# Kernel optimization log

Hardware: AMD Instinct MI355X
Metric: run time of the kernel (lower is better)

Reference implementation:

```python
import jax, jax.numpy as jnp
import numpy as np

B, NQ, NK, D, H, DK, DV, M = 1, 2048, 2048, 1024, 16, 64, 64, 64
EPS = 1e-5

def _layer_norm(x, gamma, beta):
    mu = jnp.mean(x, axis=-1, keepdims=True)
    var = jnp.mean(jnp.square(x - mu), axis=-1, keepdims=True)
    return (x - mu) * jax.lax.rsqrt(var + EPS) * gamma + beta

def setup_inputs() -> dict:
    key = jax.random.key(0)
    ks = jax.random.split(key, 16)
    s = 0.02  # xavier-ish init scale for 1024x1024 weights
    return {
        'queries': jax.random.normal(ks[0], (B, NQ, D), jnp.float32),
        'keys': jax.random.normal(ks[1], (B, NK, D), jnp.float32),
        'values': jax.random.normal(ks[2], (B, NK, D), jnp.float32),
        'attention_weights': jax.random.uniform(ks[3], (B, NQ, NK), jnp.float32),
        'prev_att': jax.random.normal(ks[4], (B, NQ, NK), jnp.float32) * 0.1,
        'attention_mask': jax.random.randint(ks[5], (B, NQ, NK), 0, 2).astype(bool),
        'Wq': jax.random.normal(ks[6], (H * DK, D), jnp.float32) * s,
        'bq': jnp.zeros((H * DK,), jnp.float32),
        'Wk': jax.random.normal(ks[7], (H * DK, D), jnp.float32) * s,
        'bk': jnp.zeros((H * DK,), jnp.float32),
        'Wv': jax.random.normal(ks[8], (H * DV, D), jnp.float32) * s,
        'bv': jnp.zeros((H * DV,), jnp.float32),
        'Wo': jax.random.normal(ks[9], (D, H * DV), jnp.float32) * s,
        'bo': jnp.zeros((D,), jnp.float32),
        'm_k': jax.random.normal(ks[10], (1, H, DK, M), jnp.float32) * s,  # stored pre-permuted as in module
        'm_v': jax.random.normal(ks[11], (1, H, M, DV), jnp.float32) * s,
        'gamma': jnp.ones((D,), jnp.float32),
        'beta': jnp.zeros((D,), jnp.float32),
    }

def reference(queries, keys, values, attention_weights, prev_att, attention_mask,
              Wq, bq, Wk, bk, Wv, bv, Wo, bo, m_k, m_v, gamma, beta):
    b, nq = queries.shape[:2]
    nk = keys.shape[1]
    # projections -> (b, h, nq, dk), (b, h, dk, nk), (b, h, nk, dv)
    q = (queries @ Wq.T + bq).reshape(b, nq, H, DK).transpose(0, 2, 1, 3)
    k = (keys @ Wk.T + bk).reshape(b, nk, H, DK).transpose(0, 2, 3, 1)
    v = (values @ Wv.T + bv).reshape(b, nk, H, DV).transpose(0, 2, 1, 3)
    # memory-slot concatenation
    k = jnp.concatenate([k, jnp.broadcast_to(m_k, (b, H, DK, M))], axis=3)   # (b,h,dk,nk+M)
    v = jnp.concatenate([v, jnp.broadcast_to(m_v, (b, H, M, DV))], axis=2)   # (b,h,nk+M,dv)
    aw = jnp.concatenate([attention_weights, jnp.ones((b, nq, M), attention_weights.dtype)], axis=-1)
    pa = jnp.concatenate([prev_att, jnp.zeros((b, nq, M), prev_att.dtype)], axis=-1)
    mask = jnp.concatenate([attention_mask, jnp.zeros((b, nq, M), bool)], axis=-1)
    # scores: scale, reweight, bias, mask (b_s==1 so rank-3 aw/pa broadcast over heads as in torch)
    att = jnp.einsum('bhqd,bhdn->bhqn', q, k) / np.sqrt(DK).astype(np.float32)
    att = att * aw + pa
    r_att = jnp.where(mask[:, None, :, :], -jnp.inf, att)
    p = jax.nn.softmax(r_att, axis=-1)  # dropout is identity (p=0 / eval)
    out = jnp.einsum('bhqn,bhnv->bqhv', p, v).reshape(b, nq, H * DV)
    out = out @ Wo.T + bo
    out = _layer_norm(queries + out, gamma, beta)  # use_res=True
    return out, r_att
```

## Files before the change

### kernel.cpp

```cpp
#include <hip/hip_runtime.h>
#include <hip/hip_bf16.h>
#include <math.h>

#define NQ 2048
#define NK 2048
#define DMODEL 1024
#define NHEAD 16
#define DK 64
#define DV 64
#define MSLOT 64
#define NKM (NK + MSLOT)
#define OUT_ELEMS (NQ * DMODEL)
#define RATT_ELEMS (NHEAD * NQ * NKM)

#define NEG_BIG (-1.0e30f)

#define LD4(p) (*(const float4*)(p))
#define ST4(p, v) (*(float4*)(p) = (v))

__device__ __forceinline__ void gemm64_body(
    const float* __restrict__ X, const float* __restrict__ W,
    const float* __restrict__ bias, float* __restrict__ C,
    int M, int N, int K, int bx, int by)
{
    __shared__ float Xs[32][68];
    __shared__ float Ws[32][68];
    const int t = threadIdx.x;
    const int ty = t >> 4, tx = t & 15;
    const int m0 = by * 64, n0 = bx * 64;
    float acc[4][4] = {};

    const int u = (t < 128) ? t : (t - 128);
    const int r4 = (u >> 3) * 4;
    const int c4 = u & 7;
    const float* src = (t < 128) ? &X[(size_t)(m0 + r4) * K + c4 * 4]
                                 : &W[(size_t)(n0 + r4) * K + c4 * 4];

    float4 v0, v1, v2, v3;
    v0 = LD4(src); v1 = LD4(src + K); v2 = LD4(src + 2 * K); v3 = LD4(src + 3 * K);

    for (int k0 = 0; k0 < K; k0 += 32) {
        __syncthreads();
        if (t < 128) {
            ST4(&Xs[c4 * 4 + 0][r4], make_float4(v0.x, v1.x, v2.x, v3.x));
            ST4(&Xs[c4 * 4 + 1][r4], make_float4(v0.y, v1.y, v2.y, v3.y));
            ST4(&Xs[c4 * 4 + 2][r4], make_float4(v0.z, v1.z, v2.z, v3.z));
            ST4(&Xs[c4 * 4 + 3][r4], make_float4(v0.w, v1.w, v2.w, v3.w));
        } else {
            ST4(&Ws[c4 * 4 + 0][r4], make_float4(v0.x, v1.x, v2.x, v3.x));
            ST4(&Ws[c4 * 4 + 1][r4], make_float4(v0.y, v1.y, v2.y, v3.y));
            ST4(&Ws[c4 * 4 + 2][r4], make_float4(v0.z, v1.z, v2.z, v3.z));
            ST4(&Ws[c4 * 4 + 3][r4], make_float4(v0.w, v1.w, v2.w, v3.w));
        }
        if (k0 + 32 < K) {
            const float* p = src + k0 + 32;
            v0 = LD4(p); v1 = LD4(p + K); v2 = LD4(p + 2 * K); v3 = LD4(p + 3 * K);
        }
        __syncthreads();
#pragma unroll 8
        for (int kk = 0; kk < 32; ++kk) {
            float a[4], b[4];
            *(float4*)&a[0] = LD4(&Xs[kk][ty * 4]);
            *(float4*)&b[0] = LD4(&Ws[kk][tx * 4]);
#pragma unroll
            for (int i = 0; i < 4; ++i)
#pragma unroll
                for (int j = 0; j < 4; ++j)
                    acc[i][j] += a[i] * b[j];
        }
    }
    float4 bv = LD4(&bias[n0 + tx * 4]);
#pragma unroll
    for (int i = 0; i < 4; ++i) {
        float4 o = make_float4(acc[i][0] + bv.x, acc[i][1] + bv.y,
                               acc[i][2] + bv.z, acc[i][3] + bv.w);
        ST4(&C[(size_t)(m0 + ty * 4 + i) * N + n0 + tx * 4], o);
    }
}

__global__ __launch_bounds__(256) void gemm64(
    const float* __restrict__ X, const float* __restrict__ W,
    const float* __restrict__ bias, float* __restrict__ C,
    int M, int N, int K)
{
    gemm64_body(X, W, bias, C, M, N, K, blockIdx.x, blockIdx.y);
}

__global__ __launch_bounds__(256) void qkv_gemm(
    const float* __restrict__ Xq, const float* __restrict__ Xk, const float* __restrict__ Xv,
    const float* __restrict__ Wq, const float* __restrict__ Wk, const float* __restrict__ Wv,
    const float* __restrict__ bq, const float* __restrict__ bk, const float* __restrict__ bv,
    float* __restrict__ Cq, float* __restrict__ Ck, float* __restrict__ Cv)
{
    const int z = blockIdx.z;
    const float* X = (z == 0) ? Xq : (z == 1) ? Xk : Xv;
    const float* W = (z == 0) ? Wq : (z == 1) ? Wk : Wv;
    const float* b = (z == 0) ? bq : (z == 1) ? bk : bv;
    float* C       = (z == 0) ? Cq : (z == 1) ? Ck : Cv;
    gemm64_body(X, W, b, C, NQ, DMODEL, DMODEL, blockIdx.x, blockIdx.y);
}

__global__ __launch_bounds__(256) void scores_main(
    const float* __restrict__ Q, const float* __restrict__ K,
    const float* __restrict__ AW, const float* __restrict__ PA,
    const unsigned char* __restrict__ MASK, float* __restrict__ Ratt)
{
    __shared__ float Qs[64][132];
    __shared__ float Ks[64][132];
    const int t = threadIdx.x;
    const int h = blockIdx.z;
    const int q0 = blockIdx.y * 128;
    const int n0 = blockIdx.x * 128;

#pragma unroll
    for (int i = 0; i < 2; ++i) {
        int idx = t + i * 256;
        int r = (idx >> 4) * 4, c4 = idx & 15;
        const float* p = &Q[(size_t)(q0 + r) * DMODEL + h * DK + c4 * 4];
        float4 v0 = LD4(p), v1 = LD4(p + DMODEL), v2 = LD4(p + 2 * DMODEL), v3 = LD4(p + 3 * DMODEL);
        ST4(&Qs[c4 * 4 + 0][r], make_float4(v0.x, v1.x, v2.x, v3.x));
        ST4(&Qs[c4 * 4 + 1][r], make_float4(v0.y, v1.y, v2.y, v3.y));
        ST4(&Qs[c4 * 4 + 2][r], make_float4(v0.z, v1.z, v2.z, v3.z));
        ST4(&Qs[c4 * 4 + 3][r], make_float4(v0.w, v1.w, v2.w, v3.w));
    }
#pragma unroll
    for (int i = 0; i < 2; ++i) {
        int idx = t + i * 256;
        int r = (idx >> 4) * 4, c4 = idx & 15;
        const float* p = &K[(size_t)(n0 + r) * DMODEL + h * DK + c4 * 4];
        float4 v0 = LD4(p), v1 = LD4(p + DMODEL), v2 = LD4(p + 2 * DMODEL), v3 = LD4(p + 3 * DMODEL);
        ST4(&Ks[c4 * 4 + 0][r], make_float4(v0.x, v1.x, v2.x, v3.x));
        ST4(&Ks[c4 * 4 + 1][r], make_float4(v0.y, v1.y, v2.y, v3.y));
        ST4(&Ks[c4 * 4 + 2][r], make_float4(v0.z, v1.z, v2.z, v3.z));
        ST4(&Ks[c4 * 4 + 3][r], make_float4(v0.w, v1.w, v2.w, v3.w));
    }
    __syncthreads();

    const int ty = t >> 4, tx = t & 15;
    float acc[8][8] = {};
#pragma unroll 4
    for (int kk = 0; kk < 64; ++kk) {
        float a[8], b[8];
        *(float4*)&a[0] = LD4(&Qs[kk][ty * 8]);
        *(float4*)&a[4] = LD4(&Qs[kk][ty * 8 + 4]);
        *(float4*)&b[0] = LD4(&Ks[kk][tx * 8]);
        *(float4*)&b[4] = LD4(&Ks[kk][tx * 8 + 4]);
#pragma unroll
        for (int i = 0; i < 8; ++i)
#pragma unroll
            for (int j = 0; j < 8; ++j)
                acc[i][j] += a[i] * b[j];
    }

#pragma unroll
    for (int i = 0; i < 8; ++i) {
        int q = q0 + ty * 8 + i;
        size_t mbase = (size_t)q * NK + n0 + tx * 8;
        size_t rbase = ((size_t)h * NQ + q) * NKM + n0 + tx * 8;
#pragma unroll
        for (int j4 = 0; j4 < 2; ++j4) {
            float4 aw = LD4(&AW[mbase + j4 * 4]);
            float4 pa = LD4(&PA[mbase + j4 * 4]);
            unsigned mm = *(const unsigned*)(MASK + mbase + j4 * 4);
            float4 o;
            o.x = (mm & 0x000000ffu) ? NEG_BIG : fmaf(acc[i][j4 * 4 + 0] * 0.125f, aw.x, pa.x);
            o.y = (mm & 0x0000ff00u) ? NEG_BIG : fmaf(acc[i][j4 * 4 + 1] * 0.125f, aw.y, pa.y);
            o.z = (mm & 0x00ff0000u) ? NEG_BIG : fmaf(acc[i][j4 * 4 + 2] * 0.125f, aw.z, pa.z);
            o.w = (mm & 0xff000000u) ? NEG_BIG : fmaf(acc[i][j4 * 4 + 3] * 0.125f, aw.w, pa.w);
            ST4(&Ratt[rbase + j4 * 4], o);
        }
    }
}

__global__ __launch_bounds__(256) void scores_mem(
    const float* __restrict__ Q, const float* __restrict__ mk,
    float* __restrict__ Ratt)
{
    __shared__ float Qs[64][132];
    __shared__ float Ks[64][68];
    const int t = threadIdx.x;
    const int h = blockIdx.y;
    const int q0 = blockIdx.x * 128;

#pragma unroll
    for (int i = 0; i < 2; ++i) {
        int idx = t + i * 256;
        int r = (idx >> 4) * 4, c4 = idx & 15;
        const float* p = &Q[(size_t)(q0 + r) * DMODEL + h * DK + c4 * 4];
        float4 v0 = LD4(p), v1 = LD4(p + DMODEL), v2 = LD4(p + 2 * DMODEL), v3 = LD4(p + 3 * DMODEL);
        ST4(&Qs[c4 * 4 + 0][r], make_float4(v0.x, v1.x, v2.x, v3.x));
        ST4(&Qs[c4 * 4 + 1][r], make_float4(v0.y, v1.y, v2.y, v3.y));
        ST4(&Qs[c4 * 4 + 2][r], make_float4(v0.z, v1.z, v2.z, v3.z));
        ST4(&Qs[c4 * 4 + 3][r], make_float4(v0.w, v1.w, v2.w, v3.w));
    }
#pragma unroll
    for (int i = 0; i < 4; ++i) {
        int idx = t + i * 256;
        int dk = idx >> 4, c4 = idx & 15;
        ST4(&Ks[dk][c4 * 4], LD4(&mk[((size_t)h * DK + dk) * MSLOT + c4 * 4]));
    }
    __syncthreads();

    const int ty = t >> 4, tx = t & 15;
    float acc[8][4] = {};
#pragma unroll 4
    for (int kk = 0; kk < 64; ++kk) {
        float a[8], b[4];
        *(float4*)&a[0] = LD4(&Qs[kk][ty * 8]);
        *(float4*)&a[4] = LD4(&Qs[kk][ty * 8 + 4]);
        *(float4*)&b[0] = LD4(&Ks[kk][tx * 4]);
#pragma unroll
        for (int i = 0; i < 8; ++i)
#pragma unroll
            for (int j = 0; j < 4; ++j)
                acc[i][j] += a[i] * b[j];
    }
#pragma unroll
    for (int i = 0; i < 8; ++i) {
        int q = q0 + ty * 8 + i;
        float4 o = make_float4(acc[i][0] * 0.125f, acc[i][1] * 0.125f,
                               acc[i][2] * 0.125f, acc[i][3] * 0.125f);
        ST4(&Ratt[((size_t)h * NQ + q) * NKM + NK + tx * 4], o);
    }
}

__global__ __launch_bounds__(256) void stats_kernel(
    const float* __restrict__ Ratt, float* __restrict__ stats)
{
    const int w = threadIdx.x >> 6, lane = threadIdx.x & 63;
    const int row = blockIdx.x * 4 + w;
    const float* r = Ratt + (size_t)row * NKM;
    float4 v[9];
#pragma unroll
    for (int i = 0; i < 8; ++i) v[i] = LD4(&r[i * 256 + lane * 4]);
    v[8] = (lane < 16) ? LD4(&r[2048 + lane * 4])
                       : make_float4(NEG_BIG, NEG_BIG, NEG_BIG, NEG_BIG);
    float m = NEG_BIG;
#pragma unroll
    for (int i = 0; i < 9; ++i)
        m = fmaxf(fmaxf(fmaxf(m, v[i].x), fmaxf(v[i].y, v[i].z)), v[i].w);
#pragma unroll
    for (int o = 32; o > 0; o >>= 1) m = fmaxf(m, __shfl_xor(m, o));
    float s = 0.f;
#pragma unroll
    for (int i = 0; i < 9; ++i)
        s += expf(v[i].x - m) + expf(v[i].y - m) + expf(v[i].z - m) + expf(v[i].w - m);
#pragma unroll
    for (int o = 32; o > 0; o >>= 1) s += __shfl_xor(s, o);
    if (lane == 0) { stats[row * 2] = m; stats[row * 2 + 1] = 1.f / s; }
}

__global__ __launch_bounds__(256) void pv_kernel(
    const float* __restrict__ Ratt, const float* __restrict__ stats,
    const float* __restrict__ V, const float* __restrict__ mv,
    float* __restrict__ AO)
{
    __shared__ float Ps[32][68];
    __shared__ float Vs[32][68];
    const int t = threadIdx.x;
    const int h = blockIdx.y;
    const int q0 = blockIdx.x * 64;
    const int ty = t >> 4, tx = t & 15;
    const int r2 = (t >> 3) * 2;
    const int n4 = t & 7;
    const int vn0 = t >> 4;
    const int vc = t & 15;

    float sm0, si0, sm1, si1;
    {
        int row = h * NQ + q0 + r2;
        sm0 = stats[row * 2];     si0 = stats[row * 2 + 1];
        sm1 = stats[row * 2 + 2]; si1 = stats[row * 2 + 3];
    }

    const float* rp = &Ratt[((size_t)h * NQ + q0 + r2) * NKM + n4 * 4];

    float4 r0 = LD4(rp), r1 = LD4(rp + NKM);
    float4 w0 = LD4(&V[(size_t)vn0 * DMODEL + h * DV + vc * 4]);
    float4 w1 = LD4(&V[(size_t)(vn0 + 16) * DMODEL + h * DV + vc * 4]);

    float acc[4][4] = {};
    for (int nc = 0; nc < NKM; nc += 32) {
        float e0x = expf(r0.x - sm0) * si0, e1x = expf(r1.x - sm1) * si1;
        float e0y = expf(r0.y - sm0) * si0, e1y = expf(r1.y - sm1) * si1;
        float e0z = expf(r0.z - sm0) * si0, e1z = expf(r1.z - sm1) * si1;
        float e0w = expf(r0.w - sm0) * si0, e1w = expf(r1.w - sm1) * si1;

        if (nc + 32 < NKM) {
            const float* p = rp + nc + 32;
            r0 = LD4(p); r1 = LD4(p + NKM);
        }

        __syncthreads();
        *(float2*)&Ps[n4 * 4 + 0][r2] = make_float2(e0x, e1x);
        *(float2*)&Ps[n4 * 4 + 1][r2] = make_float2(e0y, e1y);
        *(float2*)&Ps[n4 * 4 + 2][r2] = make_float2(e0z, e1z);
        *(float2*)&Ps[n4 * 4 + 3][r2] = make_float2(e0w, e1w);
        ST4(&Vs[vn0][vc * 4], w0);
        ST4(&Vs[vn0 + 16][vc * 4], w1);

        if (nc + 32 < NKM) {
            int ng0 = nc + 32 + vn0;
            int ng1 = nc + 32 + vn0 + 16;
            const float* vp0 = (ng0 < NK) ? &V[(size_t)ng0 * DMODEL + h * DV + vc * 4]
                                          : &mv[((size_t)h * MSLOT + (ng0 - NK)) * DV + vc * 4];
            const float* vp1 = (ng1 < NK) ? &V[(size_t)ng1 * DMODEL + h * DV + vc * 4]
                                          : &mv[((size_t)h * MSLOT + (ng1 - NK)) * DV + vc * 4];
            w0 = LD4(vp0); w1 = LD4(vp1);
        }
        __syncthreads();

#pragma unroll 8
        for (int kk = 0; kk < 32; ++kk) {
            float a[4], b[4];
            *(float4*)&a[0] = LD4(&Ps[kk][ty * 4]);
            *(float4*)&b[0] = LD4(&Vs[kk][tx * 4]);
#pragma unroll
            for (int i = 0; i < 4; ++i)
#pragma unroll
                for (int j = 0; j < 4; ++j)
                    acc[i][j] += a[i] * b[j];
        }
    }
#pragma unroll
    for (int i = 0; i < 4; ++i)
        ST4(&AO[(size_t)(q0 + ty * 4 + i) * DMODEL + h * DV + tx * 4],
            make_float4(acc[i][0], acc[i][1], acc[i][2], acc[i][3]));
}

__global__ __launch_bounds__(256) void ln_kernel(
    const float* __restrict__ Xres, const float* __restrict__ T,
    const float* __restrict__ gamma, const float* __restrict__ beta,
    float* __restrict__ out)
{
    const int row = blockIdx.x;
    const int t = threadIdx.x;
    const int w = t >> 6, lane = t & 63;
    __shared__ float red1[4], red2[4];

    float4 x = LD4(&Xres[(size_t)row * DMODEL + t * 4]);
    float4 tv = LD4(&T[(size_t)row * DMODEL + t * 4]);
    float v0 = x.x + tv.x, v1 = x.y + tv.y, v2 = x.z + tv.z, v3 = x.w + tv.w;

    float s = v0 + v1 + v2 + v3;
#pragma unroll
    for (int o = 32; o > 0; o >>= 1) s += __shfl_xor(s, o);
    if (lane == 0) red1[w] = s;
    __syncthreads();
    float mu = (red1[0] + red1[1] + red1[2] + red1[3]) * (1.f / DMODEL);

    float d0 = v0 - mu, d1 = v1 - mu, d2 = v2 - mu, d3 = v3 - mu;
    float vs = d0 * d0 + d1 * d1 + d2 * d2 + d3 * d3;
#pragma unroll
    for (int o = 32; o > 0; o >>= 1) vs += __shfl_xor(vs, o);
    if (lane == 0) red2[w] = vs;
    __syncthreads();
    float inv = rsqrtf((red2[0] + red2[1] + red2[2] + red2[3]) * (1.f / DMODEL) + 1e-5f);

    float4 g = LD4(&gamma[t * 4]);
    float4 bb = LD4(&beta[t * 4]);
    float4 o4 = make_float4(d0 * inv * g.x + bb.x, d1 * inv * g.y + bb.y,
                            d2 * inv * g.z + bb.z, d3 * inv * g.w + bb.w);
    ST4(&out[(size_t)row * DMODEL + t * 4], o4);
}

extern "C" void kernel_launch(void* const* d_in, const int* in_sizes, int n_in,
                              void* d_out, int out_size, void* d_ws, size_t ws_size,
                              hipStream_t stream) {
    const float* queries = (const float*)d_in[0];
    const float* keys    = (const float*)d_in[1];
    const float* values  = (const float*)d_in[2];
    const float* AW      = (const float*)d_in[3];
    const float* PA      = (const float*)d_in[4];
    const unsigned char* MASK = (const unsigned char*)d_in[5];
    const float* Wq = (const float*)d_in[6];  const float* bq = (const float*)d_in[7];
    const float* Wk = (const float*)d_in[8];  const float* bk = (const float*)d_in[9];
    const float* Wv = (const float*)d_in[10]; const float* bv = (const float*)d_in[11];
    const float* Wo = (const float*)d_in[12]; const float* bo = (const float*)d_in[13];
    const float* mk = (const float*)d_in[14]; const float* mv = (const float*)d_in[15];
    const float* gamma = (const float*)d_in[16]; const float* beta = (const float*)d_in[17];

    float* out  = (float*)d_out;
    float* ratt = out + OUT_ELEMS;

    float* ws = (float*)d_ws;
    float* Qp    = ws;
    float* Kp    = ws + 1 * OUT_ELEMS;
    float* Vp    = ws + 2 * OUT_ELEMS;
    float* AO    = ws + 3 * OUT_ELEMS;
    float* T     = ws + 4 * OUT_ELEMS;
    float* stats = ws + 5 * OUT_ELEMS;

    qkv_gemm<<<dim3(DMODEL / 64, NQ / 64, 3), 256, 0, stream>>>(
        queries, keys, values, Wq, Wk, Wv, bq, bk, bv, Qp, Kp, Vp);

    scores_main<<<dim3(NK / 128, NQ / 128, NHEAD), 256, 0, stream>>>(
        Qp, Kp, AW, PA, MASK, ratt);
    scores_mem<<<dim3(NQ / 128, NHEAD), 256, 0, stream>>>(Qp, mk, ratt);

    stats_kernel<<<(NHEAD * NQ) / 4, 256, 0, stream>>>(ratt, stats);

    pv_kernel<<<dim3(NQ / 64, NHEAD), 256, 0, stream>>>(ratt, stats, Vp, mv, AO);

    gemm64<<<dim3(DMODEL / 64, NQ / 64), 256, 0, stream>>>(
        AO, Wo, bo, T, NQ, DMODEL, DMODEL);

    ln_kernel<<<NQ, 256, 0, stream>>>(queries, T, gamma, beta, out);
}
```

Measured before the change: 951.4 us.

## Use bf16 MFMA for scores and PV, fuse partial softmax stats into scores

The QKV projection now writes bf16 outputs. The QK^T scores and P·V products move from scalar FP32 FMA to bf16 MFMA 16x16x32 instructions, with a new kernel that pre-transposes V into bf16. The scores kernels now emit per-tile row max and sum partials, so the separate stats pass reduces only 33 partials per row instead of rereading the whole score matrix. This removes a full read of the large r_att tensor and moves the matmul work onto matrix cores, at the cost of bf16 rounding in Q, K, V and P, which may affect accuracy.

```diff
diff --git a/kernel.cpp b/kernel.cpp
--- a/kernel.cpp
+++ b/kernel.cpp
@@ -1,5 +1,4 @@
 #include <hip/hip_runtime.h>
-#include <hip/hip_bf16.h>
 #include <math.h>
 
 #define NQ 2048
@@ -11,23 +10,44 @@
 #define MSLOT 64
 #define NKM (NK + MSLOT)
 #define OUT_ELEMS (NQ * DMODEL)
-#define RATT_ELEMS (NHEAD * NQ * NKM)
 
 #define NEG_BIG (-1.0e30f)
 
 #define LD4(p) (*(const float4*)(p))
 #define ST4(p, v) (*(float4*)(p) = (v))
 
-__device__ __forceinline__ void gemm64_body(
-    const float* __restrict__ X, const float* __restrict__ W,
-    const float* __restrict__ bias, float* __restrict__ C,
-    int M, int N, int K, int bx, int by)
-{
+using bfx8 = __attribute__((ext_vector_type(8))) short;
+using fx4  = __attribute__((ext_vector_type(4))) float;
+
+static __device__ __forceinline__ unsigned short f2bf(float f) {
+    union { float f; unsigned u; } v; v.f = f;
+    unsigned r = v.u + 0x7fffu + ((v.u >> 16) & 1u);
+    return (unsigned short)(r >> 16);
+}
+static __device__ __forceinline__ float bf2f(unsigned short u) {
+    union { unsigned u; float f; } v; v.u = (unsigned)u << 16;
+    return v.f;
+}
+
+__global__ __launch_bounds__(256) void qkv_gemm(
+    const float* __restrict__ Xq, const float* __restrict__ Xk, const float* __restrict__ Xv,
+    const float* __restrict__ Wq, const float* __restrict__ Wk, const float* __restrict__ Wv,
+    const float* __restrict__ bq, const float* __restrict__ bk, const float* __restrict__ bv,
+    unsigned short* __restrict__ Qb, unsigned short* __restrict__ Kb,
+    unsigned short* __restrict__ Vb)
+{
+    const int z = blockIdx.z;
+    const float* X = (z == 0) ? Xq : (z == 1) ? Xk : Xv;
+    const float* W = (z == 0) ? Wq : (z == 1) ? Wk : Wv;
+    const float* bias = (z == 0) ? bq : (z == 1) ? bk : bv;
+    unsigned short* O = (z == 0) ? Qb : (z == 1) ? Kb : Vb;
+
     __shared__ float Xs[32][68];
     __shared__ float Ws[32][68];
     const int t = threadIdx.x;
     const int ty = t >> 4, tx = t & 15;
-    const int m0 = by * 64, n0 = bx * 64;
+    const int m0 = blockIdx.y * 64, n0 = blockIdx.x * 64;
+    const int K = DMODEL;
     float acc[4][4] = {};
 
     const int u = (t < 128) ? t : (t - 128);
@@ -36,8 +56,7 @@
     const float* src = (t < 128) ? &X[(size_t)(m0 + r4) * K + c4 * 4]
                                  : &W[(size_t)(n0 + r4) * K + c4 * 4];
 
-    float4 v0, v1, v2, v3;
-    v0 = LD4(src); v1 = LD4(src + K); v2 = LD4(src + 2 * K); v3 = LD4(src + 3 * K);
+    float4 v0 = LD4(src), v1 = LD4(src + K), v2 = LD4(src + 2 * K), v3 = LD4(src + 3 * K);
 
     for (int k0 = 0; k0 < K; k0 += 32) {
         __syncthreads();
@@ -69,112 +88,108 @@
                     acc[i][j] += a[i] * b[j];
         }
     }
-    float4 bv = LD4(&bias[n0 + tx * 4]);
+    float4 bv4 = LD4(&bias[n0 + tx * 4]);
 #pragma unroll
     for (int i = 0; i < 4; ++i) {
-        float4 o = make_float4(acc[i][0] + bv.x, acc[i][1] + bv.y,
-                               acc[i][2] + bv.z, acc[i][3] + bv.w);
-        ST4(&C[(size_t)(m0 + ty * 4 + i) * N + n0 + tx * 4], o);
-    }
-}
-
-__global__ __launch_bounds__(256) void gemm64(
-    const float* __restrict__ X, const float* __restrict__ W,
-    const float* __restrict__ bias, float* __restrict__ C,
-    int M, int N, int K)
-{
-    gemm64_body(X, W, bias, C, M, N, K, blockIdx.x, blockIdx.y);
-}
-
-__global__ __launch_bounds__(256) void qkv_gemm(
-    const float* __restrict__ Xq, const float* __restrict__ Xk, const float* __restrict__ Xv,
-    const float* __restrict__ Wq, const float* __restrict__ Wk, const float* __restrict__ Wv,
-    const float* __restrict__ bq, const float* __restrict__ bk, const float* __restrict__ bv,
-    float* __restrict__ Cq, float* __restrict__ Ck, float* __restrict__ Cv)
-{
-    const int z = blockIdx.z;
-    const float* X = (z == 0) ? Xq : (z == 1) ? Xk : Xv;
-    const float* W = (z == 0) ? Wq : (z == 1) ? Wk : Wv;
-    const float* b = (z == 0) ? bq : (z == 1) ? bk : bv;
-    float* C       = (z == 0) ? Cq : (z == 1) ? Ck : Cv;
-    gemm64_body(X, W, b, C, NQ, DMODEL, DMODEL, blockIdx.x, blockIdx.y);
-}
-
-__global__ __launch_bounds__(256) void scores_main(
-    const float* __restrict__ Q, const float* __restrict__ K,
+        ushort4 o;
+        o.x = f2bf(acc[i][0] + bv4.x);
+        o.y = f2bf(acc[i][1] + bv4.y);
+        o.z = f2bf(acc[i][2] + bv4.z);
+        o.w = f2bf(acc[i][3] + bv4.w);
+        *(ushort4*)(O + (size_t)(m0 + ty * 4 + i) * DMODEL + n0 + tx * 4) = o;
+    }
+}
+
+__global__ __launch_bounds__(256) void vt_prep(
+    const unsigned short* __restrict__ Vb, const float* __restrict__ mv,
+    unsigned short* __restrict__ Vt)
+{
+    __shared__ unsigned short L[64][72];
+    const int c = blockIdx.x;
+    const int h = blockIdx.y;
+    const int t = threadIdx.x;
+    const int rn = t >> 2;
+    const int g4 = t & 3;
+
+    if (c < 32) {
+        const unsigned short* p = Vb + (size_t)(c * 64 + rn) * DMODEL + h * DV + g4 * 16;
+#pragma unroll
+        for (int e = 0; e < 16; ++e) L[rn][g4 * 16 + e] = p[e];
+    } else {
+        const float* p = mv + ((size_t)h * MSLOT + rn) * DV + g4 * 16;
+#pragma unroll
+        for (int e = 0; e < 16; ++e) L[rn][g4 * 16 + e] = f2bf(p[e]);
+    }
+    __syncthreads();
+    const int dv = rn;
+    unsigned short* q = Vt + ((size_t)h * DV + dv) * NKM + c * 64 + g4 * 16;
+#pragma unroll
+    for (int e = 0; e < 16; ++e) q[e] = L[g4 * 16 + e][dv];
+}
+
+__global__ __launch_bounds__(256) void scores_mfma(
+    const unsigned short* __restrict__ Qb, const unsigned short* __restrict__ Kb,
     const float* __restrict__ AW, const float* __restrict__ PA,
-    const unsigned char* __restrict__ MASK, float* __restrict__ Ratt)
-{
-    __shared__ float Qs[64][132];
-    __shared__ float Ks[64][132];
-    const int t = threadIdx.x;
+    const unsigned char* __restrict__ MASK, float* __restrict__ Ratt,
+    float2* __restrict__ pf)
+{
+    const int t = threadIdx.x;
+    const int lane = t & 63, w = t >> 6;
+    const int wq = w >> 1, wn = w & 1;
     const int h = blockIdx.z;
-    const int q0 = blockIdx.y * 128;
-    const int n0 = blockIdx.x * 128;
-
-#pragma unroll
-    for (int i = 0; i < 2; ++i) {
-        int idx = t + i * 256;
-        int r = (idx >> 4) * 4, c4 = idx & 15;
-        const float* p = &Q[(size_t)(q0 + r) * DMODEL + h * DK + c4 * 4];
-        float4 v0 = LD4(p), v1 = LD4(p + DMODEL), v2 = LD4(p + 2 * DMODEL), v3 = LD4(p + 3 * DMODEL);
-        ST4(&Qs[c4 * 4 + 0][r], make_float4(v0.x, v1.x, v2.x, v3.x));
-        ST4(&Qs[c4 * 4 + 1][r], make_float4(v0.y, v1.y, v2.y, v3.y));
-        ST4(&Qs[c4 * 4 + 2][r], make_float4(v0.z, v1.z, v2.z, v3.z));
-        ST4(&Qs[c4 * 4 + 3][r], make_float4(v0.w, v1.w, v2.w, v3.w));
-    }
-#pragma unroll
-    for (int i = 0; i < 2; ++i) {
-        int idx = t + i * 256;
-        int r = (idx >> 4) * 4, c4 = idx & 15;
-        const float* p = &K[(size_t)(n0 + r) * DMODEL + h * DK + c4 * 4];
-        float4 v0 = LD4(p), v1 = LD4(p + DMODEL), v2 = LD4(p + 2 * DMODEL), v3 = LD4(p + 3 * DMODEL);
-        ST4(&Ks[c4 * 4 + 0][r], make_float4(v0.x, v1.x, v2.x, v3.x));
-        ST4(&Ks[c4 * 4 + 1][r], make_float4(v0.y, v1.y, v2.y, v3.y));
-        ST4(&Ks[c4 * 4 + 2][r], make_float4(v0.z, v1.z, v2.z, v3.z));
-        ST4(&Ks[c4 * 4 + 3][r], make_float4(v0.w, v1.w, v2.w, v3.w));
-    }
-    __syncthreads();
-
-    const int ty = t >> 4, tx = t & 15;
-    float acc[8][8] = {};
-#pragma unroll 4
-    for (int kk = 0; kk < 64; ++kk) {
-        float a[8], b[8];
-        *(float4*)&a[0] = LD4(&Qs[kk][ty * 8]);
-        *(float4*)&a[4] = LD4(&Qs[kk][ty * 8 + 4]);
-        *(float4*)&b[0] = LD4(&Ks[kk][tx * 8]);
-        *(float4*)&b[4] = LD4(&Ks[kk][tx * 8 + 4]);
-#pragma unroll
-        for (int i = 0; i < 8; ++i)
-#pragma unroll
-            for (int j = 0; j < 8; ++j)
-                acc[i][j] += a[i] * b[j];
-    }
-
-#pragma unroll
-    for (int i = 0; i < 8; ++i) {
-        int q = q0 + ty * 8 + i;
-        size_t mbase = (size_t)q * NK + n0 + tx * 8;
-        size_t rbase = ((size_t)h * NQ + q) * NKM + n0 + tx * 8;
-#pragma unroll
-        for (int j4 = 0; j4 < 2; ++j4) {
-            float4 aw = LD4(&AW[mbase + j4 * 4]);
-            float4 pa = LD4(&PA[mbase + j4 * 4]);
-            unsigned mm = *(const unsigned*)(MASK + mbase + j4 * 4);
-            float4 o;
-            o.x = (mm & 0x000000ffu) ? NEG_BIG : fmaf(acc[i][j4 * 4 + 0] * 0.125f, aw.x, pa.x);
-            o.y = (mm & 0x0000ff00u) ? NEG_BIG : fmaf(acc[i][j4 * 4 + 1] * 0.125f, aw.y, pa.y);
-            o.z = (mm & 0x00ff0000u) ? NEG_BIG : fmaf(acc[i][j4 * 4 + 2] * 0.125f, aw.z, pa.z);
-            o.w = (mm & 0xff000000u) ? NEG_BIG : fmaf(acc[i][j4 * 4 + 3] * 0.125f, aw.w, pa.w);
-            ST4(&Ratt[rbase + j4 * 4], o);
+    const int q0 = blockIdx.y * 128, n0 = blockIdx.x * 128;
+    const int lr = lane & 15, lg = lane >> 4;
+
+    const unsigned short* qbase = Qb + (size_t)(q0 + wq * 64 + lr) * DMODEL + h * DK + lg * 8;
+    const unsigned short* kbase = Kb + (size_t)(n0 + wn * 64 + lr) * DMODEL + h * DK + lg * 8;
+
+    fx4 acc[4][4] = {};
+#pragma unroll
+    for (int kt = 0; kt < 2; ++kt) {
+        bfx8 a[4], b[4];
+#pragma unroll
+        for (int mt = 0; mt < 4; ++mt) a[mt] = *(const bfx8*)(qbase + mt * 16 * DMODEL + kt * 32);
+#pragma unroll
+        for (int nt = 0; nt < 4; ++nt) b[nt] = *(const bfx8*)(kbase + nt * 16 * DMODEL + kt * 32);
+#pragma unroll
+        for (int mt = 0; mt < 4; ++mt)
+#pragma unroll
+            for (int nt = 0; nt < 4; ++nt)
+                acc[mt][nt] = __builtin_amdgcn_mfma_f32_16x16x32_bf16(a[mt], b[nt], acc[mt][nt], 0, 0, 0);
+    }
+
+#pragma unroll
+    for (int mt = 0; mt < 4; ++mt) {
+#pragma unroll
+        for (int reg = 0; reg < 4; ++reg) {
+            const int q = q0 + wq * 64 + mt * 16 + lg * 4 + reg;
+            const size_t awb = (size_t)q * NK + n0 + wn * 64 + lr;
+            const size_t rb  = ((size_t)h * NQ + q) * NKM + n0 + wn * 64 + lr;
+            float o[4];
+#pragma unroll
+            for (int nt = 0; nt < 4; ++nt) {
+                float s = acc[mt][nt][reg] * 0.125f;
+                float aw = AW[awb + nt * 16];
+                float pa = PA[awb + nt * 16];
+                unsigned char mm = MASK[awb + nt * 16];
+                o[nt] = mm ? NEG_BIG : fmaf(s, aw, pa);
+                Ratt[rb + nt * 16] = o[nt];
+            }
+            float m = fmaxf(fmaxf(o[0], o[1]), fmaxf(o[2], o[3]));
+#pragma unroll
+            for (int x = 8; x >= 1; x >>= 1) m = fmaxf(m, __shfl_xor(m, x));
+            float s = expf(o[0] - m) + expf(o[1] - m) + expf(o[2] - m) + expf(o[3] - m);
+#pragma unroll
+            for (int x = 8; x >= 1; x >>= 1) s += __shfl_xor(s, x);
+            if (lr == 0)
+                pf[((size_t)h * NQ + q) * 33 + blockIdx.x * 2 + wn] = make_float2(m, s);
         }
     }
 }
 
 __global__ __launch_bounds__(256) void scores_mem(
-    const float* __restrict__ Q, const float* __restrict__ mk,
-    float* __restrict__ Ratt)
+    const unsigned short* __restrict__ Qb, const float* __restrict__ mk,
+    float* __restrict__ Ratt, float2* __restrict__ pf)
 {
     __shared__ float Qs[64][132];
     __shared__ float Ks[64][68];
@@ -183,15 +198,12 @@
     const int q0 = blockIdx.x * 128;
 
 #pragma unroll
-    for (int i = 0; i < 2; ++i) {
+    for (int i = 0; i < 4; ++i) {
         int idx = t + i * 256;
-        int r = (idx >> 4) * 4, c4 = idx & 15;
-        const float* p = &Q[(size_t)(q0 + r) * DMODEL + h * DK + c4 * 4];
-        float4 v0 = LD4(p), v1 = LD4(p + DMODEL), v2 = LD4(p + 2 * DMODEL), v3 = LD4(p + 3 * DMODEL);
-        ST4(&Qs[c4 * 4 + 0][r], make_float4(v0.x, v1.x, v2.x, v3.x));
-        ST4(&Qs[c4 * 4 + 1][r], make_float4(v0.y, v1.y, v2.y, v3.y));
-        ST4(&Qs[c4 * 4 + 2][r], make_float4(v0.z, v1.z, v2.z, v3.z));
-        ST4(&Qs[c4 * 4 + 3][r], make_float4(v0.w, v1.w, v2.w, v3.w));
+        int row = idx >> 3, g = idx & 7;
+        const unsigned short* p = Qb + (size_t)(q0 + row) * DMODEL + h * DK + g * 8;
+#pragma unroll
+        for (int e = 0; e < 8; ++e) Qs[g * 8 + e][row] = bf2f(p[e]);
     }
 #pragma unroll
     for (int i = 0; i < 4; ++i) {
@@ -218,103 +230,124 @@
 #pragma unroll
     for (int i = 0; i < 8; ++i) {
         int q = q0 + ty * 8 + i;
-        float4 o = make_float4(acc[i][0] * 0.125f, acc[i][1] * 0.125f,
-                               acc[i][2] * 0.125f, acc[i][3] * 0.125f);
-        ST4(&Ratt[((size_t)h * NQ + q) * NKM + NK + tx * 4], o);
-    }
-}
-
-__global__ __launch_bounds__(256) void stats_kernel(
-    const float* __restrict__ Ratt, float* __restrict__ stats)
+        float o0 = acc[i][0] * 0.125f, o1 = acc[i][1] * 0.125f;
+        float o2 = acc[i][2] * 0.125f, o3 = acc[i][3] * 0.125f;
+        ST4(&Ratt[((size_t)h * NQ + q) * NKM + NK + tx * 4], make_float4(o0, o1, o2, o3));
+        float m = fmaxf(fmaxf(o0, o1), fmaxf(o2, o3));
+#pragma unroll
+        for (int x = 8; x >= 1; x >>= 1) m = fmaxf(m, __shfl_xor(m, x));
+        float s = expf(o0 - m) + expf(o1 - m) + expf(o2 - m) + expf(o3 - m);
+#pragma unroll
+        for (int x = 8; x >= 1; x >>= 1) s += __shfl_xor(s, x);
+        if (tx == 0)
+            pf[((size_t)h * NQ + q) * 33 + 32] = make_float2(m, s);
+    }
+}
+
+__global__ __launch_bounds__(256) void stats_reduce(
+    const float2* __restrict__ pf, float* __restrict__ stats)
 {
     const int w = threadIdx.x >> 6, lane = threadIdx.x & 63;
     const int row = blockIdx.x * 4 + w;
-    const float* r = Ratt + (size_t)row * NKM;
-    float4 v[9];
-#pragma unroll
-    for (int i = 0; i < 8; ++i) v[i] = LD4(&r[i * 256 + lane * 4]);
-    v[8] = (lane < 16) ? LD4(&r[2048 + lane * 4])
-                       : make_float4(NEG_BIG, NEG_BIG, NEG_BIG, NEG_BIG);
-    float m = NEG_BIG;
-#pragma unroll
-    for (int i = 0; i < 9; ++i)
-        m = fmaxf(fmaxf(fmaxf(m, v[i].x), fmaxf(v[i].y, v[i].z)), v[i].w);
-#pragma unroll
-    for (int o = 32; o > 0; o >>= 1) m = fmaxf(m, __shfl_xor(m, o));
-    float s = 0.f;
-#pragma unroll
-    for (int i = 0; i < 9; ++i)
-        s += expf(v[i].x - m) + expf(v[i].y - m) + expf(v[i].z - m) + expf(v[i].w - m);
-#pragma unroll
-    for (int o = 32; o > 0; o >>= 1) s += __shfl_xor(s, o);
-    if (lane == 0) { stats[row * 2] = m; stats[row * 2 + 1] = 1.f / s; }
-}
-
-__global__ __launch_bounds__(256) void pv_kernel(
+    float m = NEG_BIG, s = 0.f;
+    if (lane < 33) { float2 p = pf[(size_t)row * 33 + lane]; m = p.x; s = p.y; }
+    float M = m;
+#pragma unroll
+    for (int x = 32; x >= 1; x >>= 1) M = fmaxf(M, __shfl_xor(M, x));
+    float sc = s * expf(m - M);
+#pragma unroll
+    for (int x = 32; x >= 1; x >>= 1) sc += __shfl_xor(sc, x);
+    if (lane == 0) { stats[row * 2] = M; stats[row * 2 + 1] = 1.f / sc; }
+}
+
+__global__ __launch_bounds__(256) void pv_mfma(
     const float* __restrict__ Ratt, const float* __restrict__ stats,
-    const float* __restrict__ V, const float* __restrict__ mv,
-    float* __restrict__ AO)
-{
-    __shared__ float Ps[32][68];
-    __shared__ float Vs[32][68];
-    const int t = threadIdx.x;
+    const unsigned short* __restrict__ Vt, float* __restrict__ AO)
+{
+    const int t = threadIdx.x;
+    const int lane = t & 63, w = t >> 6;
     const int h = blockIdx.y;
-    const int q0 = blockIdx.x * 64;
+    const int q0 = blockIdx.x * 64 + w * 16;
+    const int lr = lane & 15, lg = lane >> 4;
+
+    const size_t srow = (size_t)h * NQ + q0 + lr;
+    const float sm = stats[srow * 2];
+    const float si = stats[srow * 2 + 1];
+    const float* rp = Ratt + srow * NKM + lg * 8;
+    const unsigned short* vb = Vt + ((size_t)h * DV + lr) * NKM + lg * 8;
+
+    fx4 acc[4] = {};
+#pragma unroll 2
+    for (int kc = 0; kc < NKM; kc += 32) {
+        float4 r0 = LD4(rp + kc), r1 = LD4(rp + kc + 4);
+        union { unsigned short u[8]; bfx8 v; } P;
+        P.u[0] = f2bf(expf(r0.x - sm) * si);
+        P.u[1] = f2bf(expf(r0.y - sm) * si);
+        P.u[2] = f2bf(expf(r0.z - sm) * si);
+        P.u[3] = f2bf(expf(r0.w - sm) * si);
+        P.u[4] = f2bf(expf(r1.x - sm) * si);
+        P.u[5] = f2bf(expf(r1.y - sm) * si);
+        P.u[6] = f2bf(expf(r1.z - sm) * si);
+        P.u[7] = f2bf(expf(r1.w - sm) * si);
+        bfx8 b0 = *(const bfx8*)(vb + kc);
+        bfx8 b1 = *(const bfx8*)(vb + 16 * NKM + kc);
+        bfx8 b2 = *(const bfx8*)(vb + 32 * NKM + kc);
+        bfx8 b3 = *(const bfx8*)(vb + 48 * NKM + kc);
+        acc[0] = __builtin_amdgcn_mfma_f32_16x16x32_bf16(P.v, b0, acc[0], 0, 0, 0);
+        acc[1] = __builtin_amdgcn_mfma_f32_16x16x32_bf16(P.v, b1, acc[1], 0, 0, 0);
+        acc[2] = __builtin_amdgcn_mfma_f32_16x16x32_bf16(P.v, b2, acc[2], 0, 0, 0);
+        acc[3] = __builtin_amdgcn_mfma_f32_16x16x32_bf16(P.v, b3, acc[3], 0, 0, 0);
+    }
+#pragma unroll
+    for (int nt = 0; nt < 4; ++nt)
+#pragma unroll
+        for (int reg = 0; reg < 4; ++reg)
+            AO[(size_t)(q0 + lg * 4 + reg) * DMODEL + h * DV + nt * 16 + lr] = acc[nt][reg];
+}
+
+__global__ __launch_bounds__(256) void gemm64(
+    const float* __restrict__ X, const float* __restrict__ W,
+    const float* __restrict__ bias, float* __restrict__ C,
+    int M, int N, int K)
+{
+    __shared__ float Xs[32][68];
+    __shared__ float Ws[32][68];
+    const int t = threadIdx.x;
     const int ty = t >> 4, tx = t & 15;
-    const int r2 = (t >> 3) * 2;
-    const int n4 = t & 7;
-    const int vn0 = t >> 4;
-    const int vc = t & 15;
-
-    float sm0, si0, sm1, si1;
-    {
-        int row = h * NQ + q0 + r2;
-        sm0 = stats[row * 2];     si0 = stats[row * 2 + 1];
-        sm1 = stats[row * 2 + 2]; si1 = stats[row * 2 + 3];
-    }
-
-    const float* rp = &Ratt[((size_t)h * NQ + q0 + r2) * NKM + n4 * 4];
-
-    float4 r0 = LD4(rp), r1 = LD4(rp + NKM);
-    float4 w0 = LD4(&V[(size_t)vn0 * DMODEL + h * DV + vc * 4]);
-    float4 w1 = LD4(&V[(size_t)(vn0 + 16) * DMODEL + h * DV + vc * 4]);
-
+    const int m0 = blockIdx.y * 64, n0 = blockIdx.x * 64;
     float acc[4][4] = {};
-    for (int nc = 0; nc < NKM; nc += 32) {
-        float e0x = expf(r0.x - sm0) * si0, e1x = expf(r1.x - sm1) * si1;
-        float e0y = expf(r0.y - sm0) * si0, e1y = expf(r1.y - sm1) * si1;
-        float e0z = expf(r0.z - sm0) * si0, e1z = expf(r1.z - sm1) * si1;
-        float e0w = expf(r0.w - sm0) * si0, e1w = expf(r1.w - sm1) * si1;
-
-        if (nc + 32 < NKM) {
-            const float* p = rp + nc + 32;
-            r0 = LD4(p); r1 = LD4(p + NKM);
-        }
-
+
+    const int u = (t < 128) ? t : (t - 128);
+    const int r4 = (u >> 3) * 4;
+    const int c4 = u & 7;
+    const float* src = (t < 128) ? &X[(size_t)(m0 + r4) * K + c4 * 4]
+                                 : &W[(size_t)(n0 + r4) * K + c4 * 4];
+
+    float4 v0 = LD4(src), v1 = LD4(src + K), v2 = LD4(src + 2 * K), v3 = LD4(src + 3 * K);
+
+    for (int k0 = 0; k0 < K; k0 += 32) {
         __syncthreads();
-        *(float2*)&Ps[n4 * 4 + 0][r2] = make_float2(e0x, e1x);
-        *(float2*)&Ps[n4 * 4 + 1][r2] = make_float2(e0y, e1y);
-        *(float2*)&Ps[n4 * 4 + 2][r2] = make_float2(e0z, e1z);
-        *(float2*)&Ps[n4 * 4 + 3][r2] = make_float2(e0w, e1w);
-        ST4(&Vs[vn0][vc * 4], w0);
-        ST4(&Vs[vn0 + 16][vc * 4], w1);
-
-        if (nc + 32 < NKM) {
-            int ng0 = nc + 32 + vn0;
-            int ng1 = nc + 32 + vn0 + 16;
-            const float* vp0 = (ng0 < NK) ? &V[(size_t)ng0 * DMODEL + h * DV + vc * 4]
-                                          : &mv[((size_t)h * MSLOT + (ng0 - NK)) * DV + vc * 4];
-            const float* vp1 = (ng1 < NK) ? &V[(size_t)ng1 * DMODEL + h * DV + vc * 4]
-                                          : &mv[((size_t)h * MSLOT + (ng1 - NK)) * DV + vc * 4];
-            w0 = LD4(vp0); w1 = LD4(vp1);
+        if (t < 128) {
+            ST4(&Xs[c4 * 4 + 0][r4], make_float4(v0.x, v1.x, v2.x, v3.x));
+            ST4(&Xs[c4 * 4 + 1][r4], make_float4(v0.y, v1.y, v2.y, v3.y));
+            ST4(&Xs[c4 * 4 + 2][r4], make_float4(v0.z, v1.z, v2.z, v3.z));
+            ST4(&Xs[c4 * 4 + 3][r4], make_float4(v0.w, v1.w, v2.w, v3.w));
+        } else {
+            ST4(&Ws[c4 * 4 + 0][r4], make_float4(v0.x, v1.x, v2.x, v3.x));
+            ST4(&Ws[c4 * 4 + 1][r4], make_float4(v0.y, v1.y, v2.y, v3.y));
+            ST4(&Ws[c4 * 4 + 2][r4], make_float4(v0.z, v1.z, v2.z, v3.z));
+            ST4(&Ws[c4 * 4 + 3][r4], make_float4(v0.w, v1.w, v2.w, v3.w));
+        }
+        if (k0 + 32 < K) {
+            const float* p = src + k0 + 32;
+            v0 = LD4(p); v1 = LD4(p + K); v2 = LD4(p + 2 * K); v3 = LD4(p + 3 * K);
         }
         __syncthreads();
-
 #pragma unroll 8
         for (int kk = 0; kk < 32; ++kk) {
             float a[4], b[4];
-            *(float4*)&a[0] = LD4(&Ps[kk][ty * 4]);
-            *(float4*)&b[0] = LD4(&Vs[kk][tx * 4]);
+            *(float4*)&a[0] = LD4(&Xs[kk][ty * 4]);
+            *(float4*)&b[0] = LD4(&Ws[kk][tx * 4]);
 #pragma unroll
             for (int i = 0; i < 4; ++i)
 #pragma unroll
@@ -322,10 +355,13 @@
                     acc[i][j] += a[i] * b[j];
         }
     }
-#pragma unroll
-    for (int i = 0; i < 4; ++i)
-        ST4(&AO[(size_t)(q0 + ty * 4 + i) * DMODEL + h * DV + tx * 4],
-            make_float4(acc[i][0], acc[i][1], acc[i][2], acc[i][3]));
+    float4 bv = LD4(&bias[n0 + tx * 4]);
+#pragma unroll
+    for (int i = 0; i < 4; ++i) {
+        float4 o = make_float4(acc[i][0] + bv.x, acc[i][1] + bv.y,
+                               acc[i][2] + bv.z, acc[i][3] + bv.w);
+        ST4(&C[(size_t)(m0 + ty * 4 + i) * N + n0 + tx * 4], o);
+    }
 }
 
 __global__ __launch_bounds__(256) void ln_kernel(
@@ -383,24 +419,29 @@
     float* out  = (float*)d_out;
     float* ratt = out + OUT_ELEMS;
 
-    float* ws = (float*)d_ws;
-    float* Qp    = ws;
-    float* Kp    = ws + 1 * OUT_ELEMS;
-    float* Vp    = ws + 2 * OUT_ELEMS;
-    float* AO    = ws + 3 * OUT_ELEMS;
-    float* T     = ws + 4 * OUT_ELEMS;
-    float* stats = ws + 5 * OUT_ELEMS;
+    char* base = (char*)d_ws;
+    unsigned short* Qb = (unsigned short*)(base);
+    unsigned short* Kb = (unsigned short*)(base + (4u << 20));
+    unsigned short* Vb = (unsigned short*)(base + (8u << 20));
+    unsigned short* Vt = (unsigned short*)(base + (12u << 20));
+    float* AO    = (float*)(base + 16908288);
+    float* T     = (float*)(base + 25296896);
+    float* stats = (float*)(base + 33685504);
+    float2* pf   = (float2*)AO;
 
     qkv_gemm<<<dim3(DMODEL / 64, NQ / 64, 3), 256, 0, stream>>>(
-        queries, keys, values, Wq, Wk, Wv, bq, bk, bv, Qp, Kp, Vp);
-
-    scores_main<<<dim3(NK / 128, NQ / 128, NHEAD), 256, 0, stream>>>(
-        Qp, Kp, AW, PA, MASK, ratt);
-    scores_mem<<<dim3(NQ / 128, NHEAD), 256, 0, stream>>>(Qp, mk, ratt);
-
-    stats_kernel<<<(NHEAD * NQ) / 4, 256, 0, stream>>>(ratt, stats);
-
-    pv_kernel<<<dim3(NQ / 64, NHEAD), 256, 0, stream>>>(ratt, stats, Vp, mv, AO);
+        queries, keys, values, Wq, Wk, Wv, bq, bk, bv, Qb, Kb, Vb);
+
+    vt_prep<<<dim3(33, NHEAD), 256, 0, stream>>>(Vb, mv, Vt);
+
+    scores_mfma<<<dim3(NK / 128, NQ / 128, NHEAD), 256, 0, stream>>>(
+        Qb, Kb, AW, PA, MASK, ratt, pf);
+
+    scores_mem<<<dim3(NQ / 128, NHEAD), 256, 0, stream>>>(Qb, mk, ratt, pf);
+
+    stats_reduce<<<(NHEAD * NQ) / 4, 256, 0, stream>>>(pf, stats);
+
+    pv_mfma<<<dim3(NQ / 64, NHEAD), 256, 0, stream>>>(ratt, stats, Vt, AO);
 
     gemm64<<<dim3(DMODEL / 64, NQ / 64), 256, 0, stream>>>(
         AO, Wo, bo, T, NQ, DMODEL, DMODEL);
```

Result: faster. 924.7 us (-2.8%).
